# Kernel tuning notes

Measured on AMD Instinct MI355X. Metric: run time of the kernel, lower is better.

The kernel has to match this reference:

```python
import jax, jax.numpy as jnp
import numpy as np

N = 50000   # nodes
E = 800000  # edges
IN = 16     # in_channels
H = 4       # heads (gat1)
C = 32      # hidden_channels
HC = H * C  # 128
OUT = 2


def setup_inputs() -> dict:
    key = jax.random.key(0)
    ks = jax.random.split(key, 24)
    s = 0.05
    nrm = lambda k, shape, sc=s: jax.random.normal(k, shape, dtype=jnp.float32) * sc
    return {
        "x": jax.random.normal(ks[0], (N, IN), dtype=jnp.float32),
        "edge_index": jax.random.randint(ks[1], (2, E), 0, N, dtype=jnp.int32),
        "edge_attr": jax.random.uniform(ks[2], (E, 1), dtype=jnp.float32),
        # GATv2 layer 1: in=16 -> heads=4, out=32 (concat -> 128)
        "Wl1": nrm(ks[3], (HC, IN)), "bl1": jnp.zeros((HC,), jnp.float32),
        "Wr1": nrm(ks[4], (HC, IN)), "br1": jnp.zeros((HC,), jnp.float32),
        "We1": nrm(ks[5], (HC, 1)),
        "att1": nrm(ks[6], (H, C)),
        "b1": jnp.zeros((HC,), jnp.float32),
        # GATv2 layer 2: in=128 -> heads=1, out=128
        "Wl2": nrm(ks[7], (HC, HC)), "bl2": jnp.zeros((HC,), jnp.float32),
        "Wr2": nrm(ks[8], (HC, HC)), "br2": jnp.zeros((HC,), jnp.float32),
        "We2": nrm(ks[9], (HC, 1)),
        "att2": nrm(ks[10], (1, HC)),
        "b2": jnp.zeros((HC,), jnp.float32),
        # MLP head: 128 -> 32 -> 32 -> 2
        "W1": nrm(ks[11], (C, HC)), "c1": jnp.zeros((C,), jnp.float32),
        "W2": nrm(ks[12], (32, C)), "c2": jnp.zeros((32,), jnp.float32),
        "W3": nrm(ks[13], (OUT, 32)), "c3": jnp.zeros((OUT,), jnp.float32),
    }


def gatv2_layer(x, src, dst, eattr, Wl, bl, Wr, br, We, att, bias, heads, ch, n):
    # PyG GATv2Conv (add_self_loops=False, concat=True, negative_slope=0.2)
    xl = (x @ Wl.T + bl).reshape(-1, heads, ch)  # source transform [N,H,C]
    xr = (x @ Wr.T + br).reshape(-1, heads, ch)  # target transform [N,H,C]
    ef = (eattr @ We.T).reshape(-1, heads, ch)   # edge feature [E,H,C]
    m = jax.nn.leaky_relu(xl[src] + xr[dst] + ef, 0.2)   # [E,H,C]
    logits = jnp.einsum('ehc,hc->eh', m, att)            # [E,H]
    # softmax over incoming edges of each target node
    lmax = jax.ops.segment_max(logits, dst, num_segments=n)
    lmax = jnp.where(jnp.isfinite(lmax), lmax, 0.0)
    ex = jnp.exp(logits - lmax[dst])
    denom = jax.ops.segment_sum(ex, dst, num_segments=n)
    alpha = ex / denom[dst]                               # [E,H]
    out = jax.ops.segment_sum(alpha[..., None] * xl[src], dst, num_segments=n)
    return out.reshape(-1, heads * ch) + bias


def reference(x, edge_index, edge_attr,
              Wl1, bl1, Wr1, br1, We1, att1, b1,
              Wl2, bl2, Wr2, br2, We2, att2, b2,
              W1, c1, W2, c2, W3, c3):
    src, dst = edge_index[0], edge_index[1]
    n = x.shape[0]
    h = jax.nn.elu(gatv2_layer(x, src, dst, edge_attr, Wl1, bl1, Wr1, br1, We1, att1, b1, H, C, n))
    h = jax.nn.elu(gatv2_layer(h, src, dst, edge_attr, Wl2, bl2, Wr2, br2, We2, att2, b2, 1, HC, n))
    h = jax.nn.relu(h @ W1.T + c1)
    h = jax.nn.relu(h @ W2.T + c2)
    return h @ W3.T + c3
```

## Files before the change

kernel.cpp:

```cpp
#include <hip/hip_runtime.h>
#include <hip/hip_fp16.h>
#include <math.h>

#define HCDIM 128
#define LEAKY 0.2f
#define NBUCK 256
#define CHUNK 2048
#define BCAP 5120

typedef _Float16 half8 __attribute__((ext_vector_type(8)));
typedef _Float16 hh2 __attribute__((ext_vector_type(2)));
typedef float floatx4 __attribute__((ext_vector_type(4)));


__global__ void convert_w_all_kernel(const float* __restrict__ Wl1, const float* __restrict__ Wr1,
                                     __half* __restrict__ Wcat1,
                                     const float* __restrict__ Wl2, const float* __restrict__ Wr2,
                                     __half* __restrict__ Wcat2,
                                     const float* __restrict__ W1, __half* __restrict__ W1f,
                                     const float* __restrict__ W2, __half* __restrict__ W2f,
                                     int* __restrict__ bucket_cursor) {
    int i = blockIdx.x * 256 + threadIdx.x;
    if (blockIdx.x == 0) bucket_cursor[threadIdx.x] = 0;
    if (i < 8192) {
        int row = i >> 5, c = i & 31;
        float v = 0.f;
        if (c < 16) v = (row < 128) ? Wl1[row * 16 + c] : Wr1[(row - 128) * 16 + c];
        Wcat1[i] = __float2half(v);
    } else if (i < 40960) {
        int j = i - 8192;
        float v = (j < 128 * HCDIM) ? Wl2[j] : Wr2[j - 128 * HCDIM];
        Wcat2[j] = __float2half(v);
    } else if (i < 45056) {
        int j = i - 40960;
        W1f[j] = __float2half(W1[j]);
    } else if (i < 46080) {
        int j = i - 45056;
        W2f[j] = __float2half(W2[j]);
    }
}

__global__ __launch_bounds__(256) void bin_kernel(
        const int* __restrict__ src, const int* __restrict__ dst,
        const float* __restrict__ eattr, int* __restrict__ bucket_cursor,
        int2* __restrict__ binned, int E) {
    __shared__ int hist[NBUCK];
    __shared__ int hist2[NBUCK];
    __shared__ int gbase[NBUCK];
    int t = threadIdx.x;
    int e0 = blockIdx.x * CHUNK;
    int cnt = min(CHUNK, E - e0);
    hist[t] = 0;
    hist2[t] = 0;
    __syncthreads();
    for (int i = t; i < cnt; i += 256) atomicAdd(&hist[((unsigned)dst[e0 + i]) >> 8], 1);
    __syncthreads();
    if (hist[t]) gbase[t] = atomicAdd(&bucket_cursor[t], hist[t]);
    __syncthreads();
    for (int i = t; i < cnt; i += 256) {
        int d = dst[e0 + i];
        int b = ((unsigned)d) >> 8;
        unsigned sv = (unsigned)src[e0 + i] & 0xFFFFu;
        __half eh = __float2half(eattr[e0 + i]);
        int r = atomicAdd(&hist2[b], 1);
        int2 rec;
        rec.x = (int)(sv | ((unsigned)__half_as_ushort(eh) << 16));
        rec.y = d;
        binned[(size_t)b * BCAP + gbase[b] + r] = rec;
    }
}

__global__ void bucket_scan_kernel(const int* __restrict__ bucket_cursor,
                                   int* __restrict__ bucket_base) {
    __shared__ int buf[NBUCK];
    int t = threadIdx.x;
    int v = bucket_cursor[t];
    buf[t] = v;
    __syncthreads();
    for (int off = 1; off < NBUCK; off <<= 1) {
        int add = (t >= off) ? buf[t - off] : 0;
        __syncthreads();
        buf[t] += add;
        __syncthreads();
    }
    bucket_base[t] = buf[t] - v;
}

__global__ __launch_bounds__(256) void scatter2_kernel(
        const int2* __restrict__ binned, const int* __restrict__ bucket_base,
        const int* __restrict__ bucket_cursor,
        unsigned* __restrict__ packed, int* __restrict__ row_ptr, int n) {
    __shared__ int degl[NBUCK];
    __shared__ int scn[NBUCK];
    __shared__ int cur[NBUCK];
    int t = threadIdx.x;
    int b = blockIdx.x;
    int n0 = b << 8;
    int nodes = min(256, n - n0);
    size_t sbase = (size_t)b * BCAP;
    int cnt = bucket_cursor[b];
    int w0 = bucket_base[b];
    degl[t] = 0;
    __syncthreads();
    for (int i = t; i < cnt; i += 256) atomicAdd(&degl[binned[sbase + i].y & 255], 1);
    __syncthreads();
    int v = degl[t];
    scn[t] = v;
    __syncthreads();
    for (int off = 1; off < NBUCK; off <<= 1) {
        int add = (t >= off) ? scn[t - off] : 0;
        __syncthreads();
        scn[t] += add;
        __syncthreads();
    }
    int pos0 = w0 + scn[t] - v;
    cur[t] = pos0;
    if (t < nodes) row_ptr[n0 + t] = pos0;
    if (t == nodes - 1 && n0 + nodes == n) row_ptr[n] = w0 + cnt;
    __syncthreads();
    for (int i = t; i < cnt; i += 256) {
        int2 rec = binned[sbase + i];
        int p = atomicAdd(&cur[rec.y & 255], 1);
        packed[p] = (unsigned)rec.x;
    }
}

#define T16PAD 40
__global__ __launch_bounds__(256) void transform16_mfma_kernel(
        const float* __restrict__ x, const __half* __restrict__ Wcat1,
        const float* __restrict__ bl, const float* __restrict__ br,
        __half* __restrict__ xl, __half* __restrict__ xr, int n) {
    __shared__ __align__(16) __half ax[64 * T16PAD];
    int t = threadIdx.x;
    int base = blockIdx.x * 64;

    {
        int row = t >> 2, cg = t & 3;
        float4 v;
        if (base + row < n) v = *(const float4*)(x + (size_t)(base + row) * 16 + cg * 4);
        else v = make_float4(0.f, 0.f, 0.f, 0.f);
        __half2* p = (__half2*)&ax[row * T16PAD + cg * 4];
        p[0] = __floats2half2_rn(v.x, v.y);
        p[1] = __floats2half2_rn(v.z, v.w);
        __half2* z = (__half2*)&ax[row * T16PAD + 16 + cg * 4];
        z[0] = __floats2half2_rn(0.f, 0.f);
        z[1] = __floats2half2_rn(0.f, 0.f);
    }
    __syncthreads();

    int wid = t >> 6, l = t & 63;
    int lrow = l & 15, lgr = l >> 4;
    int colbase = wid * 64;

    half8 bfrag[4];
    const __half* wp = Wcat1 + (size_t)(colbase + lrow) * 32 + lgr * 8;
#pragma unroll
    for (int ct = 0; ct < 4; ++ct) bfrag[ct] = *(const half8*)(wp + ct * 16 * 32);

    float bv[4];
#pragma unroll
    for (int ct = 0; ct < 4; ++ct) {
        int col = colbase + ct * 16 + lrow;
        bv[ct] = (col < HCDIM) ? bl[col] : br[col - HCDIM];
    }
    __half* dstp = (colbase < HCDIM) ? xl : xr;
    int cb = (colbase < HCDIM) ? colbase : colbase - HCDIM;

#pragma unroll
    for (int rt = 0; rt < 4; ++rt) {
        half8 afrag = *(const half8*)&ax[(rt * 16 + lrow) * T16PAD + lgr * 8];
        floatx4 acc[4];
#pragma unroll
        for (int ct = 0; ct < 4; ++ct) {
            acc[ct] = (floatx4){0.f, 0.f, 0.f, 0.f};
            acc[ct] = __builtin_amdgcn_mfma_f32_16x16x32_f16(afrag, bfrag[ct], acc[ct], 0, 0, 0);
        }
        int rowb = base + rt * 16 + lgr * 4;
#pragma unroll
        for (int ct = 0; ct < 4; ++ct) {
            int col = cb + ct * 16 + lrow;
#pragma unroll
            for (int r = 0; r < 4; ++r) {
                int node = rowb + r;
                if (node < n) dstp[(size_t)node * HCDIM + col] = __float2half(acc[ct][r] + bv[ct]);
            }
        }
    }
}

#define TPAD 136
__global__ __launch_bounds__(256) void transform128_mfma_kernel(
        const __half* __restrict__ h, const __half* __restrict__ Wcat,
        const float* __restrict__ bl, const float* __restrict__ br,
        __half* __restrict__ xl, __half* __restrict__ xr, int n) {
    __shared__ __align__(16) __half ah[64 * TPAD];
    int t = threadIdx.x;
    int base = blockIdx.x * 64;

    for (int i = t; i < 1024; i += 256) {
        int row = i >> 4, cg = i & 15;
        uint4 v = make_uint4(0, 0, 0, 0);
        if (base + row < n) v = *(const uint4*)(h + (size_t)(base + row) * HCDIM + cg * 8);
        *(uint4*)&ah[row * TPAD + cg * 8] = v;
    }
    __syncthreads();

    int wid = t >> 6, l = t & 63;
    int lrow = l & 15, lgr = l >> 4;
    int colbase = wid * 64;

    half8 bfrag[4][4];
    const __half* wp = Wcat + (size_t)(colbase + lrow) * HCDIM + lgr * 8;
#pragma unroll
    for (int ct = 0; ct < 4; ++ct)
#pragma unroll
        for (int ks = 0; ks < 4; ++ks)
            bfrag[ct][ks] = *(const half8*)(wp + ct * 16 * HCDIM + ks * 32);

    float bv[4];
#pragma unroll
    for (int ct = 0; ct < 4; ++ct) {
        int col = colbase + ct * 16 + lrow;
        bv[ct] = (col < HCDIM) ? bl[col] : br[col - HCDIM];
    }
    __half* dstp = (colbase < HCDIM) ? xl : xr;
    int cb = (colbase < HCDIM) ? colbase : colbase - HCDIM;

#pragma unroll
    for (int rt = 0; rt < 4; ++rt) {
        half8 afrag[4];
        const __half* ap = &ah[(rt * 16 + lrow) * TPAD + lgr * 8];
#pragma unroll
        for (int ks = 0; ks < 4; ++ks) afrag[ks] = *(const half8*)(ap + ks * 32);
        floatx4 acc[4];
#pragma unroll
        for (int ct = 0; ct < 4; ++ct) {
            acc[ct] = (floatx4){0.f, 0.f, 0.f, 0.f};
#pragma unroll
            for (int ks = 0; ks < 4; ++ks)
                acc[ct] = __builtin_amdgcn_mfma_f32_16x16x32_f16(afrag[ks], bfrag[ct][ks],
                                                                 acc[ct], 0, 0, 0);
        }
        int rowb = base + rt * 16 + lgr * 4;
#pragma unroll
        for (int ct = 0; ct < 4; ++ct) {
            int col = cb + ct * 16 + lrow;
#pragma unroll
            for (int r = 0; r < 4; ++r) {
                int node = rowb + r;
                if (node < n) dstp[(size_t)node * HCDIM + col] = __float2half(acc[ct][r] + bv[ct]);
            }
        }
    }
}

template <int CTRL>
__device__ inline float dpp_radd(float x) {
    int y = __builtin_amdgcn_update_dpp(0, __float_as_int(x), CTRL, 0xF, 0xF, true);
    return x + __int_as_float(y);
}

template <int NMASK>
__device__ inline void edge_update_pk(uint4 rowbits, _Float16 eah, bool valid,
                                      const hh2* __restrict__ xr2,
                                      const hh2* __restrict__ we2,
                                      const hh2* __restrict__ at2,
                                      float& d, float* __restrict__ acc) {
    const hh2* xv2 = (const hh2*)&rowbits;
    float p = 0.f;
#pragma unroll
    for (int q = 0; q < 4; ++q) {
        hh2 m = xv2[q] + xr2[q] + eah * we2[q];
        hh2 lk = __builtin_elementwise_max(m, (_Float16)LEAKY * m);
#if __has_builtin(__builtin_amdgcn_fdot2)
        p = __builtin_amdgcn_fdot2(at2[q], lk, p, false);
#else
        p = fmaf((float)at2[q][0], (float)lk[0], fmaf((float)at2[q][1], (float)lk[1], p));
#endif
    }
    p = dpp_radd<0xB1>(p);
    p = dpp_radd<0x4E>(p);
    if constexpr (NMASK == 16) {
        p = dpp_radd<0x124>(p);
        p = dpp_radd<0x128>(p);
    }
    float w = valid ? __expf(p) : 0.f;
    d += w;
    const _Float16* xvh = (const _Float16*)&rowbits;
#pragma unroll
    for (int k = 0; k < 8; ++k) acc[k] = fmaf(w, (float)xvh[k], acc[k]);
}

__device__ inline _Float16 unpack_ea(unsigned pe) {
    ushort hb = (ushort)(pe >> 16);
    _Float16 r;
    __builtin_memcpy(&r, &hb, 2);
    return r;
}

template <int NMASK>
__global__ __launch_bounds__(256) void gat_aggregate_kernel(
        const __half* __restrict__ xl, const __half* __restrict__ xr,
        const float* __restrict__ We, const float* __restrict__ att,
        const float* __restrict__ bias,
        const unsigned* __restrict__ packed, const int* __restrict__ row_ptr,
        __half* __restrict__ hout, int n) {
    int t = threadIdx.x & 63;
    int wid = threadIdx.x >> 6;
    int g = t >> 4, u = t & 15, c0 = u * 8;
    float tmp8[8], b8[8];
    hh2 we2[4], at2[4];
    *(float4*)&tmp8[0] = *(const float4*)(We + c0);
    *(float4*)&tmp8[4] = *(const float4*)(We + c0 + 4);
#pragma unroll
    for (int q = 0; q < 4; ++q) {
        we2[q][0] = (_Float16)tmp8[2 * q];
        we2[q][1] = (_Float16)tmp8[2 * q + 1];
    }
    *(float4*)&tmp8[0] = *(const float4*)(att + c0);
    *(float4*)&tmp8[4] = *(const float4*)(att + c0 + 4);
#pragma unroll
    for (int q = 0; q < 4; ++q) {
        at2[q][0] = (_Float16)tmp8[2 * q];
        at2[q][1] = (_Float16)tmp8[2 * q + 1];
    }
    *(float4*)&b8[0] = *(const float4*)(bias + c0);
    *(float4*)&b8[4] = *(const float4*)(bias + c0 + 4);

    const __half* xlc = xl + c0;

    int node = (blockIdx.x * 4 + wid) * 4 + g;
    if (node >= n) return;

    uint4 xrbits = *(const uint4*)(xr + (size_t)node * HCDIM + c0);
    const hh2* xr2 = (const hh2*)&xrbits;
    int beg = row_ptr[node], end = row_ptr[node + 1];
    float d = 0.f, acc[8];
#pragma unroll
    for (int k = 0; k < 8; ++k) acc[k] = 0.f;
    bool has = (end > beg);
    if (has) {
        int last = end - 1;
        bool vA = true, vB = beg + 1 < end;
        bool v1A = beg + 2 < end, v1B = beg + 3 < end;
        unsigned pe0A = packed[beg];
        unsigned pe0B = packed[min(beg + 1, last)];
        unsigned pe1A = packed[min(beg + 2, last)];
        unsigned pe1B = packed[min(beg + 3, last)];
        uint4 r0A = *(const uint4*)(xlc + (size_t)(pe0A & 0xFFFFu) * HCDIM);
        uint4 r0B = *(const uint4*)(xlc + (size_t)(pe0B & 0xFFFFu) * HCDIM);
        uint4 r1A = *(const uint4*)(xlc + (size_t)(pe1A & 0xFFFFu) * HCDIM);
        uint4 r1B = *(const uint4*)(xlc + (size_t)(pe1B & 0xFFFFu) * HCDIM);
        int j = beg;
        while (true) {
            bool v2A = j + 4 < end, v2B = j + 5 < end;
            unsigned pe2A = packed[min(j + 4, last)];
            unsigned pe2B = packed[min(j + 5, last)];
            uint4 r2A = *(const uint4*)(xlc + (size_t)(pe2A & 0xFFFFu) * HCDIM);
            uint4 r2B = *(const uint4*)(xlc + (size_t)(pe2B & 0xFFFFu) * HCDIM);
            edge_update_pk<NMASK>(r0A, unpack_ea(pe0A), vA, xr2, we2, at2, d, acc);
            edge_update_pk<NMASK>(r0B, unpack_ea(pe0B), vB, xr2, we2, at2, d, acc);
            pe0A = pe1A; pe0B = pe1B; r0A = r1A; r0B = r1B; vA = v1A; vB = v1B;
            pe1A = pe2A; pe1B = pe2B; r1A = r2A; r1B = r2B; v1A = v2A; v1B = v2B;
            j += 2;
            if (!vA) break;
        }
    }

    float inv = has ? __frcp_rn(d) : 0.f;
    half8 hv;
#pragma unroll
    for (int k = 0; k < 8; ++k) {
        float v = has ? acc[k] * inv + b8[k] : b8[k];
        v = v > 0.f ? v : expm1f(v);
        hv[k] = (_Float16)v;
    }
    *(half8*)(hout + (size_t)node * HCDIM + c0) = hv;
}

#define A1S 40
__global__ __launch_bounds__(256) void mlp_head_mfma_kernel(
        const __half* __restrict__ h2, const __half* __restrict__ W1f,
        const float* __restrict__ c1, const __half* __restrict__ W2f,
        const float* __restrict__ c2, const float* __restrict__ W3,
        const float* __restrict__ c3, float* __restrict__ out, int n) {
    __shared__ __align__(16) __half hs[64 * TPAD];
    __shared__ __align__(16) __half a1[64 * A1S];
    __shared__ __align__(16) __half a2[64 * A1S];
    int t = threadIdx.x;
    int base = blockIdx.x * 64;

    for (int i = t; i < 1024; i += 256) {
        int row = i >> 4, cg = i & 15;
        uint4 v = make_uint4(0, 0, 0, 0);
        if (base + row < n) v = *(const uint4*)(h2 + (size_t)(base + row) * HCDIM + cg * 8);
        *(uint4*)&hs[row * TPAD + cg * 8] = v;
    }
    __syncthreads();

    int wid = t >> 6, l = t & 63;
    int lrow = l & 15, lgr = l >> 4;
    int rt = wid;

#pragma unroll
    for (int ct = 0; ct < 2; ++ct) {
        floatx4 acc = (floatx4){0.f, 0.f, 0.f, 0.f};
        const __half* wp = W1f + (size_t)(ct * 16 + lrow) * HCDIM + lgr * 8;
        const __half* ap = &hs[(rt * 16 + lrow) * TPAD + lgr * 8];
#pragma unroll
        for (int ks = 0; ks < 4; ++ks) {
            half8 af = *(const half8*)(ap + ks * 32);
            half8 bf = *(const half8*)(wp + ks * 32);
            acc = __builtin_amdgcn_mfma_f32_16x16x32_f16(af, bf, acc, 0, 0, 0);
        }
        int col = ct * 16 + lrow;
        float cc = c1[col];
#pragma unroll
        for (int r = 0; r < 4; ++r) {
            int row = rt * 16 + lgr * 4 + r;
            a1[row * A1S + col] = __float2half(fmaxf(acc[r] + cc, 0.f));
        }
    }
    __syncthreads();

#pragma unroll
    for (int ct = 0; ct < 2; ++ct) {
        half8 af = *(const half8*)&a1[(rt * 16 + lrow) * A1S + lgr * 8];
        half8 bf = *(const half8*)(W2f + (size_t)(ct * 16 + lrow) * 32 + lgr * 8);
        floatx4 acc = __builtin_amdgcn_mfma_f32_16x16x32_f16(af, bf,
                                                             (floatx4){0.f, 0.f, 0.f, 0.f}, 0, 0, 0);
        int col = ct * 16 + lrow;
        float cc = c2[col];
#pragma unroll
        for (int r = 0; r < 4; ++r) {
            int row = rt * 16 + lgr * 4 + r;
            a2[row * A1S + col] = __float2half(fmaxf(acc[r] + cc, 0.f));
        }
    }
    __syncthreads();

    if (t < 128) {
        int row = t >> 1, oo = t & 1;
        int node = base + row;
        if (node < n) {
            float s = c3[oo];
            const __half* ar = &a2[row * A1S];
#pragma unroll
            for (int i = 0; i < 32; ++i) s = fmaf(W3[oo * 32 + i], __half2float(ar[i]), s);
            out[(size_t)node * 2 + oo] = s;
        }
    }
}

extern "C" void kernel_launch(void* const* d_in, const int* in_sizes, int n_in,
                              void* d_out, int out_size, void* d_ws, size_t ws_size,
                              hipStream_t stream) {
    const float* x      = (const float*)d_in[0];
    const int*   eidx   = (const int*)d_in[1];
    const float* eattr  = (const float*)d_in[2];
    const float* Wl1    = (const float*)d_in[3];
    const float* bl1    = (const float*)d_in[4];
    const float* Wr1    = (const float*)d_in[5];
    const float* br1    = (const float*)d_in[6];
    const float* We1    = (const float*)d_in[7];
    const float* att1   = (const float*)d_in[8];
    const float* b1     = (const float*)d_in[9];
    const float* Wl2    = (const float*)d_in[10];
    const float* bl2    = (const float*)d_in[11];
    const float* Wr2    = (const float*)d_in[12];
    const float* br2    = (const float*)d_in[13];
    const float* We2    = (const float*)d_in[14];
    const float* att2   = (const float*)d_in[15];
    const float* b2     = (const float*)d_in[16];
    const float* W1     = (const float*)d_in[17];
    const float* c1     = (const float*)d_in[18];
    const float* W2     = (const float*)d_in[19];
    const float* c2     = (const float*)d_in[20];
    const float* W3     = (const float*)d_in[21];
    const float* c3     = (const float*)d_in[22];
    float* out = (float*)d_out;

    const int N = in_sizes[0] / 16;
    const int E = in_sizes[2];
    const int* src = eidx;
    const int* dst = eidx + E;

    char* w = (char*)d_ws;
    size_t off = 0;
    auto carve = [&](size_t bytes) -> void* {
        void* p = w + off;
        off = (off + bytes + 255) & ~(size_t)255;
        return p;
    };
    __half* xrA     = (__half*)carve((size_t)N * HCDIM * sizeof(__half));
    __half* h1      = (__half*)carve((size_t)N * HCDIM * sizeof(__half));
    __half* xlh     = (__half*)carve((size_t)N * HCDIM * sizeof(__half));
    int*    row_ptr = (int*)carve((size_t)(N + 1) * sizeof(int));
    int*    bucket_base   = (int*)carve(NBUCK * sizeof(int));
    int*    bucket_cursor = (int*)carve(NBUCK * sizeof(int));
    int2*   binned  = (int2*)carve((size_t)NBUCK * BCAP * sizeof(int2));
    unsigned* packed = (unsigned*)carve((size_t)E * sizeof(unsigned));
    __half* Wcat    = (__half*)carve((size_t)256 * HCDIM * sizeof(__half));
    __half* Wcat1   = (__half*)carve((size_t)256 * 32 * sizeof(__half));
    __half* W1f     = (__half*)carve((size_t)32 * HCDIM * sizeof(__half));
    __half* W2f     = (__half*)carve((size_t)32 * 32 * sizeof(__half));
    (void)ws_size; (void)n_in; (void)out_size;

    const int nb = (N + 255) / 256;
    const int nchunk = (E + CHUNK - 1) / CHUNK;

    convert_w_all_kernel<<<180, 256, 0, stream>>>(Wl1, Wr1, Wcat1, Wl2, Wr2, Wcat,
                                                  W1, W1f, W2, W2f, bucket_cursor);
    bin_kernel<<<nchunk, 256, 0, stream>>>(src, dst, eattr, bucket_cursor, binned, E);
    bucket_scan_kernel<<<1, 256, 0, stream>>>(bucket_cursor, bucket_base);
    scatter2_kernel<<<nb, 256, 0, stream>>>(binned, bucket_base, bucket_cursor,
                                            packed, row_ptr, N);

    transform16_mfma_kernel<<<(N + 63) / 64, 256, 0, stream>>>(
        x, Wcat1, bl1, br1, xlh, xrA, N);
    gat_aggregate_kernel<4><<<(N + 15) / 16, 256, 0, stream>>>(
        xlh, xrA, We1, att1, b1, packed, row_ptr, h1, N);

    transform128_mfma_kernel<<<(N + 63) / 64, 256, 0, stream>>>(
        h1, Wcat, bl2, br2, xlh, xrA, N);
    gat_aggregate_kernel<16><<<(N + 15) / 16, 256, 0, stream>>>(
        xlh, xrA, We2, att2, b2, packed, row_ptr, h1, N);

    mlp_head_mfma_kernel<<<(N + 63) / 64, 256, 0, stream>>>(
        h1, W1f, c1, W2f, c2, W3, c3, out, N);
}
```

Before: 257.0 us.

## Fuse GAT aggregation with following transform and MLP head, inline bucket scan

Layer-1 aggregation is fused with the layer-2 128-wide MFMA transform, and layer-2 aggregation is fused with the MLP head. The intermediate h1/h2 tiles now stay in shared memory instead of round-tripping through global memory. The single-block bucket scan is folded into scatter2, so every block recomputes the prefix scan. Together this removes three launches and two full N×128 half-precision write/read passes. In exchange, weight fragments are reloaded per 16-node block instead of per 64, and only two of four waves do work in the MLP part.

Result: faster. 251.7 us (-2.0%).

```diff
diff --git a/kernel.cpp b/kernel.cpp
--- a/kernel.cpp
+++ b/kernel.cpp
@@ -7,6 +7,8 @@
 #define NBUCK 256
 #define CHUNK 2048
 #define BCAP 5120
+#define TPAD 136
+#define A1S 40
 
 typedef _Float16 half8 __attribute__((ext_vector_type(8)));
 typedef _Float16 hh2 __attribute__((ext_vector_type(2)));
@@ -70,26 +72,10 @@
     }
 }
 
-__global__ void bucket_scan_kernel(const int* __restrict__ bucket_cursor,
-                                   int* __restrict__ bucket_base) {
-    __shared__ int buf[NBUCK];
-    int t = threadIdx.x;
-    int v = bucket_cursor[t];
-    buf[t] = v;
-    __syncthreads();
-    for (int off = 1; off < NBUCK; off <<= 1) {
-        int add = (t >= off) ? buf[t - off] : 0;
-        __syncthreads();
-        buf[t] += add;
-        __syncthreads();
-    }
-    bucket_base[t] = buf[t] - v;
-}
-
 __global__ __launch_bounds__(256) void scatter2_kernel(
-        const int2* __restrict__ binned, const int* __restrict__ bucket_base,
-        const int* __restrict__ bucket_cursor,
+        const int2* __restrict__ binned, const int* __restrict__ bucket_cursor,
         unsigned* __restrict__ packed, int* __restrict__ row_ptr, int n) {
+    __shared__ int bsc[NBUCK];
     __shared__ int degl[NBUCK];
     __shared__ int scn[NBUCK];
     __shared__ int cur[NBUCK];
@@ -99,9 +85,16 @@
     int nodes = min(256, n - n0);
     size_t sbase = (size_t)b * BCAP;
     int cnt = bucket_cursor[b];
-    int w0 = bucket_base[b];
+    bsc[t] = bucket_cursor[t];
     degl[t] = 0;
     __syncthreads();
+    for (int off = 1; off < NBUCK; off <<= 1) {
+        int add = (t >= off) ? bsc[t - off] : 0;
+        __syncthreads();
+        bsc[t] += add;
+        __syncthreads();
+    }
+    int w0 = bsc[b] - cnt;
     for (int i = t; i < cnt; i += 256) atomicAdd(&degl[binned[sbase + i].y & 255], 1);
     __syncthreads();
     int v = degl[t];
@@ -188,72 +181,6 @@
     }
 }
 
-#define TPAD 136
-__global__ __launch_bounds__(256) void transform128_mfma_kernel(
-        const __half* __restrict__ h, const __half* __restrict__ Wcat,
-        const float* __restrict__ bl, const float* __restrict__ br,
-        __half* __restrict__ xl, __half* __restrict__ xr, int n) {
-    __shared__ __align__(16) __half ah[64 * TPAD];
-    int t = threadIdx.x;
-    int base = blockIdx.x * 64;
-
-    for (int i = t; i < 1024; i += 256) {
-        int row = i >> 4, cg = i & 15;
-        uint4 v = make_uint4(0, 0, 0, 0);
-        if (base + row < n) v = *(const uint4*)(h + (size_t)(base + row) * HCDIM + cg * 8);
-        *(uint4*)&ah[row * TPAD + cg * 8] = v;
-    }
-    __syncthreads();
-
-    int wid = t >> 6, l = t & 63;
-    int lrow = l & 15, lgr = l >> 4;
-    int colbase = wid * 64;
-
-    half8 bfrag[4][4];
-    const __half* wp = Wcat + (size_t)(colbase + lrow) * HCDIM + lgr * 8;
-#pragma unroll
-    for (int ct = 0; ct < 4; ++ct)
-#pragma unroll
-        for (int ks = 0; ks < 4; ++ks)
-            bfrag[ct][ks] = *(const half8*)(wp + ct * 16 * HCDIM + ks * 32);
-
-    float bv[4];
-#pragma unroll
-    for (int ct = 0; ct < 4; ++ct) {
-        int col = colbase + ct * 16 + lrow;
-        bv[ct] = (col < HCDIM) ? bl[col] : br[col - HCDIM];
-    }
-    __half* dstp = (colbase < HCDIM) ? xl : xr;
-    int cb = (colbase < HCDIM) ? colbase : colbase - HCDIM;
-
-#pragma unroll
-    for (int rt = 0; rt < 4; ++rt) {
-        half8 afrag[4];
-        const __half* ap = &ah[(rt * 16 + lrow) * TPAD + lgr * 8];
-#pragma unroll
-        for (int ks = 0; ks < 4; ++ks) afrag[ks] = *(const half8*)(ap + ks * 32);
-        floatx4 acc[4];
-#pragma unroll
-        for (int ct = 0; ct < 4; ++ct) {
-            acc[ct] = (floatx4){0.f, 0.f, 0.f, 0.f};
-#pragma unroll
-            for (int ks = 0; ks < 4; ++ks)
-                acc[ct] = __builtin_amdgcn_mfma_f32_16x16x32_f16(afrag[ks], bfrag[ct][ks],
-                                                                 acc[ct], 0, 0, 0);
-        }
-        int rowb = base + rt * 16 + lgr * 4;
-#pragma unroll
-        for (int ct = 0; ct < 4; ++ct) {
-            int col = cb + ct * 16 + lrow;
-#pragma unroll
-            for (int r = 0; r < 4; ++r) {
-                int node = rowb + r;
-                if (node < n) dstp[(size_t)node * HCDIM + col] = __float2half(acc[ct][r] + bv[ct]);
-            }
-        }
-    }
-}
-
 template <int CTRL>
 __device__ inline float dpp_radd(float x) {
     int y = __builtin_amdgcn_update_dpp(0, __float_as_int(x), CTRL, 0xF, 0xF, true);
@@ -299,46 +226,22 @@
 }
 
 template <int NMASK>
-__global__ __launch_bounds__(256) void gat_aggregate_kernel(
-        const __half* __restrict__ xl, const __half* __restrict__ xr,
-        const float* __restrict__ We, const float* __restrict__ att,
-        const float* __restrict__ bias,
-        const unsigned* __restrict__ packed, const int* __restrict__ row_ptr,
-        __half* __restrict__ hout, int n) {
-    int t = threadIdx.x & 63;
-    int wid = threadIdx.x >> 6;
-    int g = t >> 4, u = t & 15, c0 = u * 8;
-    float tmp8[8], b8[8];
-    hh2 we2[4], at2[4];
-    *(float4*)&tmp8[0] = *(const float4*)(We + c0);
-    *(float4*)&tmp8[4] = *(const float4*)(We + c0 + 4);
-#pragma unroll
-    for (int q = 0; q < 4; ++q) {
-        we2[q][0] = (_Float16)tmp8[2 * q];
-        we2[q][1] = (_Float16)tmp8[2 * q + 1];
-    }
-    *(float4*)&tmp8[0] = *(const float4*)(att + c0);
-    *(float4*)&tmp8[4] = *(const float4*)(att + c0 + 4);
-#pragma unroll
-    for (int q = 0; q < 4; ++q) {
-        at2[q][0] = (_Float16)tmp8[2 * q];
-        at2[q][1] = (_Float16)tmp8[2 * q + 1];
-    }
-    *(float4*)&b8[0] = *(const float4*)(bias + c0);
-    *(float4*)&b8[4] = *(const float4*)(bias + c0 + 4);
-
-    const __half* xlc = xl + c0;
-
-    int node = (blockIdx.x * 4 + wid) * 4 + g;
-    if (node >= n) return;
-
-    uint4 xrbits = *(const uint4*)(xr + (size_t)node * HCDIM + c0);
+__device__ inline half8 aggregate_node(int node, int n,
+                                       const __half* __restrict__ xlc,
+                                       const __half* __restrict__ xr, int c0,
+                                       const unsigned* __restrict__ packed,
+                                       const int* __restrict__ row_ptr,
+                                       const hh2* __restrict__ we2,
+                                       const hh2* __restrict__ at2,
+                                       const float* __restrict__ b8) {
+    int nodec = min(node, n - 1);
+    uint4 xrbits = *(const uint4*)(xr + (size_t)nodec * HCDIM + c0);
     const hh2* xr2 = (const hh2*)&xrbits;
-    int beg = row_ptr[node], end = row_ptr[node + 1];
+    int beg = row_ptr[nodec], end = row_ptr[nodec + 1];
     float d = 0.f, acc[8];
 #pragma unroll
     for (int k = 0; k < 8; ++k) acc[k] = 0.f;
-    bool has = (end > beg);
+    bool has = (node < n) && (end > beg);
     if (has) {
         int last = end - 1;
         bool vA = true, vB = beg + 1 < end;
@@ -366,7 +269,6 @@
             if (!vA) break;
         }
     }
-
     float inv = has ? __frcp_rn(d) : 0.f;
     half8 hv;
 #pragma unroll
@@ -375,38 +277,130 @@
         v = v > 0.f ? v : expm1f(v);
         hv[k] = (_Float16)v;
     }
-    *(half8*)(hout + (size_t)node * HCDIM + c0) = hv;
-}
-
-#define A1S 40
-__global__ __launch_bounds__(256) void mlp_head_mfma_kernel(
-        const __half* __restrict__ h2, const __half* __restrict__ W1f,
-        const float* __restrict__ c1, const __half* __restrict__ W2f,
-        const float* __restrict__ c2, const float* __restrict__ W3,
-        const float* __restrict__ c3, float* __restrict__ out, int n) {
-    __shared__ __align__(16) __half hs[64 * TPAD];
-    __shared__ __align__(16) __half a1[64 * A1S];
-    __shared__ __align__(16) __half a2[64 * A1S];
+    return hv;
+}
+
+__device__ inline void load_edge_consts(const float* We, const float* att,
+                                        const float* bias, int c0,
+                                        hh2* we2, hh2* at2, float* b8) {
+    float tmp8[8];
+    *(float4*)&tmp8[0] = *(const float4*)(We + c0);
+    *(float4*)&tmp8[4] = *(const float4*)(We + c0 + 4);
+#pragma unroll
+    for (int q = 0; q < 4; ++q) {
+        we2[q][0] = (_Float16)tmp8[2 * q];
+        we2[q][1] = (_Float16)tmp8[2 * q + 1];
+    }
+    *(float4*)&tmp8[0] = *(const float4*)(att + c0);
+    *(float4*)&tmp8[4] = *(const float4*)(att + c0 + 4);
+#pragma unroll
+    for (int q = 0; q < 4; ++q) {
+        at2[q][0] = (_Float16)tmp8[2 * q];
+        at2[q][1] = (_Float16)tmp8[2 * q + 1];
+    }
+    *(float4*)&b8[0] = *(const float4*)(bias + c0);
+    *(float4*)&b8[4] = *(const float4*)(bias + c0 + 4);
+}
+
+__global__ __launch_bounds__(256) void gat_agg1_t128_kernel(
+        const __half* __restrict__ xl, const __half* __restrict__ xr,
+        const float* __restrict__ We, const float* __restrict__ att,
+        const float* __restrict__ bias,
+        const unsigned* __restrict__ packed, const int* __restrict__ row_ptr,
+        const __half* __restrict__ Wcat, const float* __restrict__ bl2,
+        const float* __restrict__ br2,
+        __half* __restrict__ xl2, __half* __restrict__ xr2, int n) {
+    __shared__ __align__(16) __half hs[16 * TPAD];
     int t = threadIdx.x;
-    int base = blockIdx.x * 64;
-
-    for (int i = t; i < 1024; i += 256) {
-        int row = i >> 4, cg = i & 15;
-        uint4 v = make_uint4(0, 0, 0, 0);
-        if (base + row < n) v = *(const uint4*)(h2 + (size_t)(base + row) * HCDIM + cg * 8);
-        *(uint4*)&hs[row * TPAD + cg * 8] = v;
-    }
-    __syncthreads();
-
-    int wid = t >> 6, l = t & 63;
-    int lrow = l & 15, lgr = l >> 4;
-    int rt = wid;
-
-#pragma unroll
-    for (int ct = 0; ct < 2; ++ct) {
+    int tl = t & 63, wid = t >> 6;
+    int g = tl >> 4, u = tl & 15, c0 = u * 8;
+    hh2 we2[4], at2[4];
+    float b8[8];
+    load_edge_consts(We, att, bias, c0, we2, at2, b8);
+
+    int base = blockIdx.x * 16;
+    int rel = wid * 4 + g;
+    int node = base + rel;
+    half8 hv = aggregate_node<4>(node, n, xl + c0, xr, c0, packed, row_ptr, we2, at2, b8);
+    *(half8*)&hs[rel * TPAD + c0] = hv;
+    __syncthreads();
+
+    int lrow = tl & 15, lgr = tl >> 4;
+    int colbase = wid * 64;
+    half8 bfrag[4][4];
+    const __half* wp = Wcat + (size_t)(colbase + lrow) * HCDIM + lgr * 8;
+#pragma unroll
+    for (int ct = 0; ct < 4; ++ct)
+#pragma unroll
+        for (int ks = 0; ks < 4; ++ks)
+            bfrag[ct][ks] = *(const half8*)(wp + ct * 16 * HCDIM + ks * 32);
+
+    float bv[4];
+#pragma unroll
+    for (int ct = 0; ct < 4; ++ct) {
+        int col = colbase + ct * 16 + lrow;
+        bv[ct] = (col < HCDIM) ? bl2[col] : br2[col - HCDIM];
+    }
+    __half* dstp = (colbase < HCDIM) ? xl2 : xr2;
+    int cb = (colbase < HCDIM) ? colbase : colbase - HCDIM;
+
+    half8 afrag[4];
+    const __half* ap = &hs[lrow * TPAD + lgr * 8];
+#pragma unroll
+    for (int ks = 0; ks < 4; ++ks) afrag[ks] = *(const half8*)(ap + ks * 32);
+    floatx4 acc[4];
+#pragma unroll
+    for (int ct = 0; ct < 4; ++ct) {
+        acc[ct] = (floatx4){0.f, 0.f, 0.f, 0.f};
+#pragma unroll
+        for (int ks = 0; ks < 4; ++ks)
+            acc[ct] = __builtin_amdgcn_mfma_f32_16x16x32_f16(afrag[ks], bfrag[ct][ks],
+                                                             acc[ct], 0, 0, 0);
+    }
+    int rowb = base + lgr * 4;
+#pragma unroll
+    for (int ct = 0; ct < 4; ++ct) {
+        int col = cb + ct * 16 + lrow;
+#pragma unroll
+        for (int r = 0; r < 4; ++r) {
+            int node2 = rowb + r;
+            if (node2 < n) dstp[(size_t)node2 * HCDIM + col] = __float2half(acc[ct][r] + bv[ct]);
+        }
+    }
+}
+
+__global__ __launch_bounds__(256) void gat_agg2_mlp_kernel(
+        const __half* __restrict__ xl, const __half* __restrict__ xr,
+        const float* __restrict__ We, const float* __restrict__ att,
+        const float* __restrict__ bias,
+        const unsigned* __restrict__ packed, const int* __restrict__ row_ptr,
+        const __half* __restrict__ W1f, const float* __restrict__ c1,
+        const __half* __restrict__ W2f, const float* __restrict__ c2,
+        const float* __restrict__ W3, const float* __restrict__ c3,
+        float* __restrict__ out, int n) {
+    __shared__ __align__(16) __half hs[16 * TPAD];
+    __shared__ __align__(16) __half a1[16 * A1S];
+    __shared__ __align__(16) __half a2[16 * A1S];
+    int t = threadIdx.x;
+    int tl = t & 63, wid = t >> 6;
+    int g = tl >> 4, u = tl & 15, c0 = u * 8;
+    hh2 we2[4], at2[4];
+    float b8[8];
+    load_edge_consts(We, att, bias, c0, we2, at2, b8);
+
+    int base = blockIdx.x * 16;
+    int rel = wid * 4 + g;
+    int node = base + rel;
+    half8 hv = aggregate_node<16>(node, n, xl + c0, xr, c0, packed, row_ptr, we2, at2, b8);
+    *(half8*)&hs[rel * TPAD + c0] = hv;
+    __syncthreads();
+
+    int lrow = tl & 15, lgr = tl >> 4;
+    if (wid < 2) {
+        int ct = wid;
         floatx4 acc = (floatx4){0.f, 0.f, 0.f, 0.f};
         const __half* wp = W1f + (size_t)(ct * 16 + lrow) * HCDIM + lgr * 8;
-        const __half* ap = &hs[(rt * 16 + lrow) * TPAD + lgr * 8];
+        const __half* ap = &hs[lrow * TPAD + lgr * 8];
 #pragma unroll
         for (int ks = 0; ks < 4; ++ks) {
             half8 af = *(const half8*)(ap + ks * 32);
@@ -416,38 +410,32 @@
         int col = ct * 16 + lrow;
         float cc = c1[col];
 #pragma unroll
-        for (int r = 0; r < 4; ++r) {
-            int row = rt * 16 + lgr * 4 + r;
-            a1[row * A1S + col] = __float2half(fmaxf(acc[r] + cc, 0.f));
-        }
-    }
-    __syncthreads();
-
-#pragma unroll
-    for (int ct = 0; ct < 2; ++ct) {
-        half8 af = *(const half8*)&a1[(rt * 16 + lrow) * A1S + lgr * 8];
+        for (int r = 0; r < 4; ++r)
+            a1[(lgr * 4 + r) * A1S + col] = __float2half(fmaxf(acc[r] + cc, 0.f));
+    }
+    __syncthreads();
+    if (wid < 2) {
+        int ct = wid;
+        half8 af = *(const half8*)&a1[lrow * A1S + lgr * 8];
         half8 bf = *(const half8*)(W2f + (size_t)(ct * 16 + lrow) * 32 + lgr * 8);
         floatx4 acc = __builtin_amdgcn_mfma_f32_16x16x32_f16(af, bf,
                                                              (floatx4){0.f, 0.f, 0.f, 0.f}, 0, 0, 0);
         int col = ct * 16 + lrow;
         float cc = c2[col];
 #pragma unroll
-        for (int r = 0; r < 4; ++r) {
-            int row = rt * 16 + lgr * 4 + r;
-            a2[row * A1S + col] = __float2half(fmaxf(acc[r] + cc, 0.f));
-        }
-    }
-    __syncthreads();
-
-    if (t < 128) {
-        int row = t >> 1, oo = t & 1;
-        int node = base + row;
-        if (node < n) {
+        for (int r = 0; r < 4; ++r)
+            a2[(lgr * 4 + r) * A1S + col] = __float2half(fmaxf(acc[r] + cc, 0.f));
+    }
+    __syncthreads();
+    if (t < 32) {
+        int rel3 = t >> 1, oo = t & 1;
+        int node3 = base + rel3;
+        if (node3 < n) {
             float s = c3[oo];
-            const __half* ar = &a2[row * A1S];
+            const __half* ar = &a2[rel3 * A1S];
 #pragma unroll
             for (int i = 0; i < 32; ++i) s = fmaf(W3[oo * 32 + i], __half2float(ar[i]), s);
-            out[(size_t)node * 2 + oo] = s;
+            out[(size_t)node3 * 2 + oo] = s;
         }
     }
 }
@@ -492,11 +480,11 @@
         off = (off + bytes + 255) & ~(size_t)255;
         return p;
     };
-    __half* xrA     = (__half*)carve((size_t)N * HCDIM * sizeof(__half));
-    __half* h1      = (__half*)carve((size_t)N * HCDIM * sizeof(__half));
-    __half* xlh     = (__half*)carve((size_t)N * HCDIM * sizeof(__half));
+    __half* xl1     = (__half*)carve((size_t)N * HCDIM * sizeof(__half));
+    __half* xr1     = (__half*)carve((size_t)N * HCDIM * sizeof(__half));
+    __half* xl2     = (__half*)carve((size_t)N * HCDIM * sizeof(__half));
+    __half* xr2     = (__half*)carve((size_t)N * HCDIM * sizeof(__half));
     int*    row_ptr = (int*)carve((size_t)(N + 1) * sizeof(int));
-    int*    bucket_base   = (int*)carve(NBUCK * sizeof(int));
     int*    bucket_cursor = (int*)carve(NBUCK * sizeof(int));
     int2*   binned  = (int2*)carve((size_t)NBUCK * BCAP * sizeof(int2));
     unsigned* packed = (unsigned*)carve((size_t)E * sizeof(unsigned));
@@ -512,20 +500,14 @@
     convert_w_all_kernel<<<180, 256, 0, stream>>>(Wl1, Wr1, Wcat1, Wl2, Wr2, Wcat,
                                                   W1, W1f, W2, W2f, bucket_cursor);
     bin_kernel<<<nchunk, 256, 0, stream>>>(src, dst, eattr, bucket_cursor, binned, E);
-    bucket_scan_kernel<<<1, 256, 0, stream>>>(bucket_cursor, bucket_base);
-    scatter2_kernel<<<nb, 256, 0, stream>>>(binned, bucket_base, bucket_cursor,
-                                            packed, row_ptr, N);
+    scatter2_kernel<<<nb, 256, 0, stream>>>(binned, bucket_cursor, packed, row_ptr, N);
 
     transform16_mfma_kernel<<<(N + 63) / 64, 256, 0, stream>>>(
-        x, Wcat1, bl1, br1, xlh, xrA, N);
-    gat_aggregate_kernel<4><<<(N + 15) / 16, 256, 0, stream>>>(
-        xlh, xrA, We1, att1, b1, packed, row_ptr, h1, N);
-
-    transform128_mfma_kernel<<<(N + 63) / 64, 256, 0, stream>>>(
-        h1, Wcat, bl2, br2, xlh, xrA, N);
-    gat_aggregate_kernel<16><<<(N + 15) / 16, 256, 0, stream>>>(
-        xlh, xrA, We2, att2, b2, packed, row_ptr, h1, N);
-
-    mlp_head_mfma_kernel<<<(N + 63) / 64, 256, 0, stream>>>(
-        h1, W1f, c1, W2f, c2, W3, c3, out, N);
-}
+        x, Wcat1, bl1, br1, xl1, xr1, N);
+
+    gat_agg1_t128_kernel<<<(N + 15) / 16, 256, 0, stream>>>(
+        xl1, xr1, We1, att1, b1, packed, row_ptr, Wcat, bl2, br2, xl2, xr2, N);
+
+    gat_agg2_mlp_kernel<<<(N + 15) / 16, 256, 0, stream>>>(
+        xl2, xr2, We2, att2, b2, packed, row_ptr, W1f, c1, W2f, c2, W3, c3, out, N);
+}
```
